# Optimization experiments

Measured on AMD Instinct MI355X. Metric: run time of the kernel, lower is better.

Reference implementation:

```python
import jax, jax.numpy as jnp
import numpy as np

NEG, NEG2, EPS, K = 0.01, 0.2, 1e-5, 10
B, N = 8, 2048

def lrelu(x, s):
    return jnp.where(x >= 0, x, s * x)

def bn_eval(x, g, b):
    # BatchNorm in eval mode with running_mean=0, running_var=1
    shp = [1] * x.ndim; shp[1] = -1
    return x * (g / np.sqrt(1.0 + EPS)).reshape(shp) + b.reshape(shp)

def conv1d(x, W, b):  # x [B,C,N], W [O,C]
    return jnp.einsum('bcn,oc->bon', x, W) + b[None, :, None]

def conv2d_1x1(x, W, b):  # x [B,C,N,K], W [O,C]
    return jnp.einsum('bcnk,oc->bonk', x, W) + b[None, :, None, None]

def edge_feats(x, k):
    # x: [B, d, N] -> [B, 2d, N, k]
    xt = jnp.swapaxes(x, 1, 2)                                   # [B,N,d]
    dist = (-2.0 * jnp.einsum('bnd,bdm->bnm', xt, x)
            + jnp.sum(xt ** 2, axis=2, keepdims=True)
            + jnp.sum(x ** 2, axis=1, keepdims=True))            # [B,N,N]
    idx = jnp.argsort(dist, axis=2)[:, :, 1:k + 1]               # [B,N,k]
    nbrs = jax.vmap(lambda xb, ib: xb[:, ib])(x, idx)            # [B,d,N,k]
    c = x[:, :, :, None]
    return jnp.concatenate([jnp.broadcast_to(c, nbrs.shape), nbrs - c], axis=1)

def edge_block(x, wc1, wcb1, bn1g, bn1b, wc2, wcb2, bn2g, bn2b,
               xc, xcb, xbng, xbnb, oW, ob):
    C = x.shape[1]
    ee = edge_feats(x, K)                                        # [B,2C,N,K]
    w = lrelu(bn_eval(conv2d_1x1(ee[:, C:], wc1, wcb1), bn1g, bn1b), NEG)
    w = lrelu(bn_eval(conv2d_1x1(w, wc2, wcb2), bn2g, bn2b), NEG)
    w = jax.nn.softmax(w, axis=-1)
    h = lrelu(bn_eval(conv2d_1x1(ee, xc, xcb), xbng, xbnb), NEG)
    # Conv2d(Fout, Fout, [1,K]): contract channels and neighbor axis
    return jnp.einsum('bcnj,ocj->bon', h * w, oW) + ob[None, :, None]

def adain(x, style, W, b):
    s = conv1d(style, W, b)
    g, be = jnp.split(s, 2, axis=1)
    m = jnp.mean(x, axis=2, keepdims=True)
    v = jnp.mean((x - m) ** 2, axis=2, keepdims=True)
    return g * ((x - m) * jax.lax.rsqrt(v + EPS)) + be

def _forward(z, x, hW1, hb1, hW2, hb2,
             e1_wc1, e1_wcb1, e1_bn1g, e1_bn1b, e1_wc2, e1_wcb2, e1_bn2g, e1_bn2b,
             e1_xc, e1_xcb, e1_xbng, e1_xbnb, e1_oW, e1_ob, a1_W, a1_b,
             e2_wc1, e2_wcb1, e2_bn1g, e2_bn1b, e2_wc2, e2_wcb2, e2_bn2g, e2_bn2b,
             e2_xc, e2_xcb, e2_xbng, e2_xbnb, e2_oW, e2_ob, a2_W, a2_b,
             gW1, gb1, gbn1g, gbn1b, gW2, gb2, gbn2g, gbn2b,
             tW1, tb1, tW2, tb2, tW3, tb3):
    st = jnp.swapaxes(jnp.concatenate([x, z], axis=-1), 1, 2)    # [B,3+nz,N]
    st = lrelu(conv1d(st, hW1, hb1), NEG)
    st = lrelu(conv1d(st, hW2, hb2), NEG)                        # [B,128,N]
    pc = jnp.swapaxes(x, 1, 2)                                   # [B,3,N]
    x1 = edge_block(pc, e1_wc1, e1_wcb1, e1_bn1g, e1_bn1b, e1_wc2, e1_wcb2,
                    e1_bn2g, e1_bn2b, e1_xc, e1_xcb, e1_xbng, e1_xbnb, e1_oW, e1_ob)
    x1 = adain(lrelu(x1, NEG2), st, a1_W, a1_b)                  # [B,64,N]
    x2 = edge_block(x1, e2_wc1, e2_wcb1, e2_bn1g, e2_bn1b, e2_wc2, e2_wcb2,
                    e2_bn2g, e2_bn2b, e2_xc, e2_xcb, e2_xbng, e2_xbnb, e2_oW, e2_ob)
    x2 = adain(lrelu(x2, NEG2), st, a2_W, a2_b)                  # [B,128,N]
    fg = jnp.max(x2, axis=2)                                     # [B,128]
    fg = lrelu(bn_eval(fg @ gW1.T + gb1, gbn1g, gbn1b), NEG)
    fg = lrelu(bn_eval(fg @ gW2.T + gb2, gbn2g, gbn2b), NEG)     # [B,512]
    fg = jnp.broadcast_to(fg[:, :, None], (fg.shape[0], 512, x2.shape[2]))
    feat = jnp.concatenate([fg, x2], axis=1)                     # [B,640,N]
    t = lrelu(conv1d(feat, tW1, tb1), NEG)
    t = lrelu(conv1d(t, tW2, tb2), NEG)
    t = conv1d(t, tW3, tb3)
    return jnp.swapaxes(t, 1, 2)                                 # [B,N,3]

_PARAM_SPECS = [
    ('hW1', (128, 131)), ('hb1', (128,)), ('hW2', (128, 128)), ('hb2', (128,)),
    ('e1_wc1', (32, 3)), ('e1_wcb1', (32,)), ('e1_bn1g', (32,)), ('e1_bn1b', (32,)),
    ('e1_wc2', (64, 32)), ('e1_wcb2', (64,)), ('e1_bn2g', (64,)), ('e1_bn2b', (64,)),
    ('e1_xc', (64, 6)), ('e1_xcb', (64,)), ('e1_xbng', (64,)), ('e1_xbnb', (64,)),
    ('e1_oW', (64, 64, 10)), ('e1_ob', (64,)), ('a1_W', (128, 128)), ('a1_b', (128,)),
    ('e2_wc1', (64, 64)), ('e2_wcb1', (64,)), ('e2_bn1g', (64,)), ('e2_bn1b', (64,)),
    ('e2_wc2', (128, 64)), ('e2_wcb2', (128,)), ('e2_bn2g', (128,)), ('e2_bn2b', (128,)),
    ('e2_xc', (128, 128)), ('e2_xcb', (128,)), ('e2_xbng', (128,)), ('e2_xbnb', (128,)),
    ('e2_oW', (128, 128, 10)), ('e2_ob', (128,)), ('a2_W', (256, 128)), ('a2_b', (256,)),
    ('gW1', (128, 128)), ('gb1', (128,)), ('gbn1g', (128,)), ('gbn1b', (128,)),
    ('gW2', (512, 128)), ('gb2', (512,)), ('gbn2g', (512,)), ('gbn2b', (512,)),
    ('tW1', (256, 640)), ('tb1', (256,)), ('tW2', (64, 256)), ('tb2', (64,)),
    ('tW3', (3, 64)), ('tb3', (3,)),
]

def setup_inputs() -> dict:
    key = jax.random.key(0)
    d = {
        'z': jax.random.normal(jax.random.fold_in(key, 1000), (B, N, 128), jnp.float32),
        'x': jax.random.normal(jax.random.fold_in(key, 1001), (B, N, 3), jnp.float32),
    }
    for i, (nm, sh) in enumerate(_PARAM_SPECS):
        v = 0.1 * jax.random.normal(jax.random.fold_in(key, i), sh, jnp.float32)
        if nm.endswith('g'):  # batchnorm gammas around 1
            v = v + 1.0
        d[nm] = v
    return d

def reference(z, x, hW1, hb1, hW2, hb2,
              e1_wc1, e1_wcb1, e1_bn1g, e1_bn1b, e1_wc2, e1_wcb2, e1_bn2g, e1_bn2b,
              e1_xc, e1_xcb, e1_xbng, e1_xbnb, e1_oW, e1_ob, a1_W, a1_b,
              e2_wc1, e2_wcb1, e2_bn1g, e2_bn1b, e2_wc2, e2_wcb2, e2_bn2g, e2_bn2b,
              e2_xc, e2_xcb, e2_xbng, e2_xbnb, e2_oW, e2_ob, a2_W, a2_b,
              gW1, gb1, gbn1g, gbn1b, gW2, gb2, gbn2g, gbn2b,
              tW1, tb1, tW2, tb2, tW3, tb3):
    return _forward(z, x, hW1, hb1, hW2, hb2,
                    e1_wc1, e1_wcb1, e1_bn1g, e1_bn1b, e1_wc2, e1_wcb2, e1_bn2g, e1_bn2b,
                    e1_xc, e1_xcb, e1_xbng, e1_xbnb, e1_oW, e1_ob, a1_W, a1_b,
                    e2_wc1, e2_wcb1, e2_bn1g, e2_bn1b, e2_wc2, e2_wcb2, e2_bn2g, e2_bn2b,
                    e2_xc, e2_xcb, e2_xbng, e2_xbnb, e2_oW, e2_ob, a2_W, a2_b,
                    gW1, gb1, gbn1g, gbn1b, gW2, gb2, gbn2g, gbn2b,
                    tW1, tb1, tW2, tb2, tW3, tb3)
```

## Files before the change

kernel.cpp:

```cpp
#include <hip/hip_runtime.h>
#include <math.h>

#define NPTS 2048
#define BATCH 8
#define KNB 10
#define NT (NPTS*KNB)

static __device__ __forceinline__ float lrelu(float x, float s){ return x >= 0.f ? x : s*x; }
static __device__ __forceinline__ double lrelu_d(double x, double s){ return x >= 0.0 ? x : s*x; }

template<int TM, int TN>
__global__ __launch_bounds__(256) void gemm_bn(
    const float* __restrict__ In, int ldn, size_t inBS, int koff,
    const float* __restrict__ W, int wstride, int wcol0,
    const float* __restrict__ cb, const float* __restrict__ bng, const float* __restrict__ bnb,
    const float* __restrict__ addBO, int addM,
    float* __restrict__ Out, int ldo, size_t outBS,
    int C, int act, float neg, int bbase)
{
  constexpr int RM = TM/16, RN = TN/16;
  __shared__ float As[16][TM+4];
  __shared__ float Bs[16][TN+4];
  const int b = bbase + blockIdx.z;
  const float* in = In + (size_t)b*inBS;
  float* outp = Out + (size_t)b*outBS;
  const int m0 = blockIdx.y*TM, n0 = blockIdx.x*TN;
  const int t = threadIdx.x;
  const int tmv = t>>4, tnv = t&15;
  float acc[RM][RN] = {};
  for (int k0=0; k0<C; k0+=16){
    #pragma unroll
    for (int s=0;s<RM;s++){
      const int i = t + s*256;
      const int k = i&15, m = i>>4;
      As[k][m] = W[(size_t)(m0+m)*wstride + wcol0 + k0 + k];
    }
    #pragma unroll
    for (int s=0;s<RN;s++){
      const int i = t + s*256;
      const int n = i & (TN-1), kk2 = i / TN;
      Bs[kk2][n] = in[(size_t)(koff + k0 + kk2)*ldn + n0 + n];
    }
    __syncthreads();
    #pragma unroll
    for (int kk=0;kk<16;kk++){
      float av[RM], bv[RN];
      #pragma unroll
      for (int s=0;s<RM/4;s++){
        float4 v = *(const float4*)&As[kk][tmv*RM + s*4];
        av[s*4]=v.x; av[s*4+1]=v.y; av[s*4+2]=v.z; av[s*4+3]=v.w;
      }
      #pragma unroll
      for (int s=0;s<RN/4;s++){
        float4 v = *(const float4*)&Bs[kk][tnv*RN + s*4];
        bv[s*4]=v.x; bv[s*4+1]=v.y; bv[s*4+2]=v.z; bv[s*4+3]=v.w;
      }
      #pragma unroll
      for (int i2=0;i2<RM;i2++)
        #pragma unroll
        for (int j2=0;j2<RN;j2++) acc[i2][j2] += av[i2]*bv[j2];
    }
    __syncthreads();
  }
  const float rs = 1.f/sqrtf(1.f + 1e-5f);
  #pragma unroll
  for (int i2=0;i2<RM;i2++){
    const int gm = m0 + tmv*RM + i2;
    float addv = cb ? cb[gm] : 0.f;
    if (addBO) addv += addBO[b*addM + gm];
    float sc = 1.f, bs = 0.f;
    if (bng){ sc = bng[gm]*rs; bs = bnb[gm]; }
    float* orow = outp + (size_t)gm*ldo + n0 + tnv*RN;
    #pragma unroll
    for (int j4=0;j4<RN/4;j4++){
      float4 o;
      float vv[4];
      #pragma unroll
      for (int q=0;q<4;q++){
        float v = acc[i2][j4*4+q] + addv;
        if (bng) v = v*sc + bs;
        if (act) v = lrelu(v, neg);
        vv[q] = v;
      }
      o.x=vv[0]; o.y=vv[1]; o.z=vv[2]; o.w=vv[3];
      *(float4*)&orow[j4*4] = o;
    }
  }
}

__global__ __launch_bounds__(256) void conv_gemm_exact(
    const float* __restrict__ in, const float* __restrict__ W, int wstride, int wcol0,
    const float* __restrict__ bias,
    float* __restrict__ out, int C, int M, int act, float neg)
{
  __shared__ float As[16][68];
  __shared__ float Bs[16][68];
  const int b = blockIdx.z;
  const int m0 = blockIdx.y*64, n0 = blockIdx.x*64;
  const int t = threadIdx.x;
  const int tm = t>>4, tn = t&15;
  float acc[4][4] = {};
  for (int k0 = 0; k0 < C; k0 += 16){
    #pragma unroll
    for (int i=0;i<4;i++){
      const int ii = t + i*256;
      const int k = ii&15, m = ii>>4;
      const int gm = m0+m, gk = k0+k;
      As[k][m] = (gm<M && gk<C) ? W[(size_t)gm*wstride + wcol0 + gk] : 0.f;
    }
    #pragma unroll
    for (int i=0;i<4;i++){
      const int ii = t + i*256;
      const int n = ii&63, k = ii>>6;
      const int gk = k0+k;
      Bs[k][n] = (gk<C) ? in[((size_t)b*C+gk)*NPTS + n0+n] : 0.f;
    }
    __syncthreads();
    #pragma unroll
    for (int k=0;k<16;k++){
      #pragma unroll
      for (int i=0;i<4;i++){
        const float a = As[k][tm*4+i];
        #pragma unroll
        for (int j=0;j<4;j++){
          acc[i][j] = __fadd_rn(acc[i][j], __fmul_rn(a, Bs[k][tn*4+j]));
        }
      }
    }
    __syncthreads();
  }
  #pragma unroll
  for (int i=0;i<4;i++){
    const int gm = m0 + tm*4 + i;
    if (gm < M){
      const float bv = bias ? bias[gm] : 0.f;
      #pragma unroll
      for (int j=0;j<4;j++){
        float v = __fadd_rn(acc[i][j], bv);
        if (act) v = (v >= 0.f) ? v : __fmul_rn(neg, v);
        out[((size_t)b*M+gm)*NPTS + n0 + tn*4 + j] = v;
      }
    }
  }
}

__global__ __launch_bounds__(256) void head1_exact(
    const float* __restrict__ x, const float* __restrict__ z,
    const float* __restrict__ W, const float* __restrict__ bias,
    float* __restrict__ outh)
{
  __shared__ float As[16][68];
  __shared__ float Bs[16][68];
  const int b = blockIdx.z;
  const int m0 = blockIdx.y*64, n0 = blockIdx.x*64;
  const int t = threadIdx.x;
  const int tm = t>>4, tn = t&15;
  float acc[4][4] = {};
  for (int k0 = 0; k0 < 144; k0 += 16){
    #pragma unroll
    for (int i=0;i<4;i++){
      const int ii = t + i*256;
      const int k = ii&15, m = ii>>4;
      const int gk = k0+k;
      As[k][m] = (gk<131) ? W[(size_t)(m0+m)*131 + gk] : 0.f;
    }
    #pragma unroll
    for (int i=0;i<4;i++){
      const int ii = t + i*256;
      const int k = ii&15, nn = ii>>4;
      const int gk = k0+k, gn = n0+nn;
      float v = 0.f;
      if (gk < 3)        v = x[((size_t)b*NPTS+gn)*3   + gk];
      else if (gk < 131) v = z[((size_t)b*NPTS+gn)*128 + (gk-3)];
      Bs[k][nn] = v;
    }
    __syncthreads();
    #pragma unroll
    for (int k=0;k<16;k++){
      #pragma unroll
      for (int i=0;i<4;i++){
        const float a = As[k][tm*4+i];
        #pragma unroll
        for (int j=0;j<4;j++){
          acc[i][j] = __fadd_rn(acc[i][j], __fmul_rn(a, Bs[k][tn*4+j]));
        }
      }
    }
    __syncthreads();
  }
  #pragma unroll
  for (int i=0;i<4;i++){
    const int gm = m0 + tm*4 + i;
    #pragma unroll
    for (int j=0;j<4;j++){
      float v = __fadd_rn(acc[i][j], bias[gm]);
      v = (v >= 0.f) ? v : __fmul_rn(0.01f, v);
      outh[((size_t)b*128+gm)*NPTS + n0 + tn*4 + j] = v;
    }
  }
}

__global__ __launch_bounds__(256) void norms3_f32(const float* __restrict__ Xn, float* __restrict__ XN)
{
  const int q = blockIdx.x*256 + threadIdx.x;
  const float* p = Xn + (size_t)q*3;
  float s = __fmul_rn(p[0],p[0]);
  s = __fadd_rn(s, __fmul_rn(p[1],p[1]));
  s = __fadd_rn(s, __fmul_rn(p[2],p[2]));
  XN[q] = s;
}

__global__ __launch_bounds__(256) void knn_part3(
    const float* __restrict__ Xn, const float* __restrict__ XN,
    double* __restrict__ topd, int* __restrict__ topi)
{
  const int t = threadIdx.x;
  const int qloc = t & 31, part = t >> 5;
  const int q = blockIdx.x*32 + qloc;
  const int b = q >> 11, n = q & (NPTS-1);
  const float* xb = Xn + (size_t)b*NPTS*3;
  const float qx = xb[(size_t)n*3+0], qy = xb[(size_t)n*3+1], qz = xb[(size_t)n*3+2];
  const float qn = XN[q];
  float td[11]; int ti[11];
  #pragma unroll
  for (int r=0;r<11;r++){ td[r] = 3.4e38f; ti[r] = 0x7fffffff; }
  const int m0 = part*(NPTS/8);
  for (int mm=0; mm<NPTS/8; mm++){
    const int m = m0 + mm;
    float dot = __fmul_rn(qx, xb[(size_t)m*3+0]);
    dot = __fadd_rn(dot, __fmul_rn(qy, xb[(size_t)m*3+1]));
    dot = __fadd_rn(dot, __fmul_rn(qz, xb[(size_t)m*3+2]));
    float dist = __fmul_rn(-2.f, dot);
    dist = __fadd_rn(dist, qn);
    dist = __fadd_rn(dist, XN[b*NPTS + m]);
    if (dist < td[10]){
      td[10] = dist; ti[10] = m;
      #pragma unroll
      for (int p=10;p>0;p--){
        if (td[p] < td[p-1]){
          float tf=td[p]; td[p]=td[p-1]; td[p-1]=tf;
          int   tt=ti[p]; ti[p]=ti[p-1]; ti[p-1]=tt;
        }
      }
    }
  }
  const size_t base = ((size_t)q*8 + part)*11;
  #pragma unroll
  for (int r=0;r<11;r++){ topd[base+r] = (double)td[r]; topi[base+r] = ti[r]; }
}

__global__ __launch_bounds__(256) void knn_merge_kernel(
    const double* __restrict__ topd, const int* __restrict__ topi, int* __restrict__ idxout)
{
  const int q = blockIdx.x*256 + threadIdx.x;
  double td[11]; int ti[11];
  #pragma unroll
  for (int r=0;r<11;r++){ td[r] = 1.0e308; ti[r] = 0x7fffffff; }
  const size_t base = (size_t)q*88;
  for (int s=0; s<88; s++){
    const double d = topd[base+s];
    const int  im = topi[base+s];
    if (d < td[10] || (d == td[10] && im < ti[10])){
      td[10] = d; ti[10] = im;
      #pragma unroll
      for (int p=10;p>0;p--){
        const bool sw = (td[p] < td[p-1]) || (td[p] == td[p-1] && ti[p] < ti[p-1]);
        if (sw){
          double tf=td[p]; td[p]=td[p-1]; td[p-1]=tf;
          int    tt=ti[p]; ti[p]=ti[p-1]; ti[p-1]=tt;
        }
      }
    }
  }
  #pragma unroll
  for (int j=0;j<KNB;j++) idxout[(size_t)q*KNB + j] = ti[j+1];
}

__global__ __launch_bounds__(256) void norms64_f32(const float* __restrict__ Xn, float* __restrict__ XN)
{
  const int q = blockIdx.x*256 + threadIdx.x;
  const float4* p4 = (const float4*)(Xn + (size_t)q*64);
  float s0=0.f,s1=0.f,s2=0.f,s3=0.f;
  #pragma unroll
  for (int d4=0; d4<16; d4++){
    float4 v = p4[d4];
    s0 += v.x*v.x; s1 += v.y*v.y; s2 += v.z*v.z; s3 += v.w*v.w;
  }
  XN[q] = (s0+s1)+(s2+s3);
}

__global__ __launch_bounds__(256) void knn_coarse(
    const float* __restrict__ Xn, const float* __restrict__ XN,
    float* __restrict__ topf, int* __restrict__ topi)
{
  const int t = threadIdx.x;
  const int qloc = t & 31, part = t >> 5;
  const int q = blockIdx.x*32 + qloc;
  const int b = q >> 11, n = q & (NPTS-1);
  const float* xb = Xn + (size_t)b*NPTS*64;
  float qv[64];
  {
    const float4* p4 = (const float4*)(xb + (size_t)n*64);
    #pragma unroll
    for (int d4=0; d4<16; d4++){ float4 v = p4[d4]; qv[d4*4]=v.x; qv[d4*4+1]=v.y; qv[d4*4+2]=v.z; qv[d4*4+3]=v.w; }
  }
  const float qn = XN[q];
  float td[16]; int ti[16];
  #pragma unroll
  for (int r=0;r<16;r++){ td[r] = 3.4e38f; ti[r] = 0x7fffffff; }
  const int m0 = part*(NPTS/8);
  #pragma unroll 2
  for (int mm=0; mm<NPTS/8; mm++){
    const int m = m0 + mm;
    const float4* c4 = (const float4*)(xb + (size_t)m*64);
    float d0=0.f,d1=0.f,d2=0.f,d3=0.f;
    #pragma unroll
    for (int d4=0; d4<16; d4++){
      float4 v = c4[d4];
      d0 += qv[d4*4+0]*v.x; d1 += qv[d4*4+1]*v.y;
      d2 += qv[d4*4+2]*v.z; d3 += qv[d4*4+3]*v.w;
    }
    const float dist = qn - 2.f*((d0+d1)+(d2+d3)) + XN[b*NPTS + m];
    if (dist < td[15]){
      td[15] = dist; ti[15] = m;
      #pragma unroll
      for (int p=15;p>0;p--){
        if (td[p] < td[p-1]){
          float tf=td[p]; td[p]=td[p-1]; td[p-1]=tf;
          int   tt=ti[p]; ti[p]=ti[p-1]; ti[p-1]=tt;
        }
      }
    }
  }
  const size_t base = ((size_t)q*8 + part)*16;
  #pragma unroll
  for (int r=0;r<16;r++){ topf[base+r] = td[r]; topi[base+r] = ti[r]; }
}

__global__ __launch_bounds__(256) void norms64d(const double* __restrict__ Xn, double* __restrict__ XN)
{
  const int q = blockIdx.x*256 + threadIdx.x;
  const double* p = Xn + (size_t)q*64;
  double s = 0.0;
  #pragma unroll
  for (int d=0; d<64; d++) s += p[d]*p[d];
  XN[q] = s;
}

__global__ __launch_bounds__(256) void knn_refine(
    const float* __restrict__ topf, const int* __restrict__ topi,
    const double* __restrict__ Xd, const double* __restrict__ XNd,
    int* __restrict__ idxout)
{
  const int q = blockIdx.x*256 + threadIdx.x;
  const int b = q >> 11;
  float tf[16]; int ti[16];
  #pragma unroll
  for (int r=0;r<16;r++){ tf[r] = 3.4e38f; ti[r] = 0x7fffffff; }
  const size_t base = (size_t)q*128;
  for (int s=0; s<128; s++){
    const float d = topf[base+s];
    const int  im = topi[base+s];
    if (d < tf[15] || (d == tf[15] && im < ti[15])){
      tf[15] = d; ti[15] = im;
      #pragma unroll
      for (int p=15;p>0;p--){
        const bool sw = (tf[p] < tf[p-1]) || (tf[p] == tf[p-1] && ti[p] < ti[p-1]);
        if (sw){
          float a=tf[p]; tf[p]=tf[p-1]; tf[p-1]=a;
          int   c=ti[p]; ti[p]=ti[p-1]; ti[p-1]=c;
        }
      }
    }
  }
  double qv[64];
  {
    const double2* p2 = (const double2*)(Xd + (size_t)q*64);
    #pragma unroll
    for (int d2=0; d2<32; d2++){ double2 v = p2[d2]; qv[d2*2]=v.x; qv[d2*2+1]=v.y; }
  }
  const double qn = XNd[q];
  double dd[11]; int di[11];
  #pragma unroll
  for (int r=0;r<11;r++){ dd[r] = 1.0e308; di[r] = 0x7fffffff; }
  for (int s=0; s<16; s++){
    const int m = ti[s];
    const double2* c2 = (const double2*)(Xd + ((size_t)(b*NPTS + m))*64);
    double d0=0.0,d1=0.0,d2s=0.0,d3=0.0;
    #pragma unroll
    for (int d4=0; d4<16; d4++){
      double2 va = c2[d4*2], vb = c2[d4*2+1];
      d0 += qv[d4*4+0]*va.x; d1 += qv[d4*4+1]*va.y;
      d2s+= qv[d4*4+2]*vb.x; d3 += qv[d4*4+3]*vb.y;
    }
    const double dot = (d0+d1)+(d2s+d3);
    const double dist = (qn - 2.0*dot) + XNd[b*NPTS + m];
    if (dist < dd[10] || (dist == dd[10] && m < di[10])){
      dd[10] = dist; di[10] = m;
      #pragma unroll
      for (int p=10;p>0;p--){
        const bool sw = (dd[p] < dd[p-1]) || (dd[p] == dd[p-1] && di[p] < di[p-1]);
        if (sw){
          double a=dd[p]; dd[p]=dd[p-1]; dd[p-1]=a;
          int    c=di[p]; di[p]=di[p-1]; di[p-1]=c;
        }
      }
    }
  }
  #pragma unroll
  for (int j=0;j<KNB;j++) idxout[(size_t)q*KNB + j] = di[j+1];
}

__global__ __launch_bounds__(512) void edge1_f64(
    const float* __restrict__ Xn, const int* __restrict__ idx,
    const float* __restrict__ wc1, const float* __restrict__ wcb1,
    const float* __restrict__ bn1g, const float* __restrict__ bn1b,
    const float* __restrict__ wc2, const float* __restrict__ wcb2,
    const float* __restrict__ bn2g, const float* __restrict__ bn2b,
    const float* __restrict__ xc,  const float* __restrict__ xcb,
    const float* __restrict__ xbng, const float* __restrict__ xbnb,
    const float* __restrict__ oWT, const float* __restrict__ ob,
    double* __restrict__ outX)
{
  __shared__ float wc1s[32][3];
  __shared__ float wc2s[64][33];
  __shared__ float xcs[64][7];
  __shared__ float wcb1s[32], wcb2s[64], xcbs[64];
  __shared__ double fs1d[32], fb1d[32], fs2d[64], fb2d[64], fsxd[64], fbxd[64];
  __shared__ float cenb[8][3], difb[8][3];
  __shared__ double w1bd[8][32];
  __shared__ float smw2[4096];
  __shared__ double hwbd[8][64];

  const int t = threadIdx.x;
  const double sq = sqrt(1.0 + 1e-5);
  for (int i=t; i<96;   i+=512) wc1s[i/3][i%3] = wc1[i];
  for (int i=t; i<2048; i+=512) wc2s[i/32][i%32] = wc2[i];
  for (int i=t; i<384;  i+=512) xcs[i/6][i%6] = xc[i];
  if (t < 32){ wcb1s[t]=wcb1[t]; fs1d[t]=(double)bn1g[t]/sq; fb1d[t]=(double)bn1b[t]; }
  else if (t < 96){ int o=t-32; wcb2s[o]=wcb2[o]; fs2d[o]=(double)bn2g[o]/sq; fb2d[o]=(double)bn2b[o]; }
  else if (t < 160){ int o=t-96; xcbs[o]=xcb[o]; fsxd[o]=(double)xbng[o]/sq; fbxd[o]=(double)xbnb[o]; }
  __syncthreads();

  const int wid = t>>6, lane = t&63;
  const int p = blockIdx.x*8 + wid;
  const int b = p >> 11, n = p & (NPTS-1);
  const float* xb = Xn + (size_t)b*NPTS*3;
  if (lane < 3) cenb[wid][lane] = xb[(size_t)n*3 + lane];
  __builtin_amdgcn_wave_barrier();
  const int* ip = idx + ((size_t)b*NPTS + n)*KNB;

  double w2r[KNB], hr[KNB];
  #pragma unroll
  for (int j=0;j<KNB;j++){
    const int id = ip[j];
    if (lane < 3) difb[wid][lane] = __fadd_rn(xb[(size_t)id*3 + lane], -cenb[wid][lane]);
    __builtin_amdgcn_wave_barrier();
    if (lane < 32){
      float s = __fmul_rn(wc1s[lane][0], difb[wid][0]);
      s = __fadd_rn(s, __fmul_rn(wc1s[lane][1], difb[wid][1]));
      s = __fadd_rn(s, __fmul_rn(wc1s[lane][2], difb[wid][2]));
      s = __fadd_rn(s, wcb1s[lane]);
      const double y = (double)s * fs1d[lane] + fb1d[lane];
      w1bd[wid][lane] = lrelu_d(y, 0.01);
    }
    __builtin_amdgcn_wave_barrier();
    {
      const int o = lane;
      double s2 = 0.0;
      #pragma unroll 8
      for (int m=0;m<32;m++) s2 += (double)wc2s[o][m] * w1bd[wid][m];
      s2 += (double)wcb2s[o];
      w2r[j] = lrelu_d(s2*fs2d[o] + fb2d[o], 0.01);
      float s3 = __fmul_rn(xcs[o][0], cenb[wid][0]);
      s3 = __fadd_rn(s3, __fmul_rn(xcs[o][1], cenb[wid][1]));
      s3 = __fadd_rn(s3, __fmul_rn(xcs[o][2], cenb[wid][2]));
      s3 = __fadd_rn(s3, __fmul_rn(xcs[o][3], difb[wid][0]));
      s3 = __fadd_rn(s3, __fmul_rn(xcs[o][4], difb[wid][1]));
      s3 = __fadd_rn(s3, __fmul_rn(xcs[o][5], difb[wid][2]));
      s3 = __fadd_rn(s3, xcbs[o]);
      hr[j] = lrelu_d((double)s3*fsxd[o] + fbxd[o], 0.01);
    }
    __builtin_amdgcn_wave_barrier();
  }

  double hw[KNB];
  {
    double mx = w2r[0];
    #pragma unroll
    for (int j=1;j<KNB;j++) mx = fmax(mx, w2r[j]);
    double ssum = 0.0;
    #pragma unroll
    for (int j=0;j<KNB;j++){ const double e = exp(w2r[j]-mx); w2r[j]=e; ssum+=e; }
    #pragma unroll
    for (int j=0;j<KNB;j++) hw[j] = hr[j]*(w2r[j]/ssum);
  }

  double acc = 0.0;
  #pragma unroll
  for (int j=0;j<KNB;j++){
    __syncthreads();
    for (int i=t; i<4096; i+=512) smw2[i] = oWT[(size_t)j*4096 + i];
    hwbd[wid][lane] = hw[j];
    __syncthreads();
    double s = 0.0;
    #pragma unroll 8
    for (int c=0;c<64;c++) s += (double)smw2[c*64 + lane]*hwbd[wid][c];
    acc += s;
  }
  outX[((size_t)b*64+lane)*NPTS + n] = acc + (double)ob[lane];
}

template<int CH>
__global__ void owt_kernel(const float* __restrict__ oW, float* __restrict__ oWT)
{
  const int i = blockIdx.x*256 + threadIdx.x;
  if (i < CH*CH*KNB){
    const int j  = i % KNB;
    const int c2 = (i / KNB) % CH;
    const int o  = i / (KNB*CH);
    oWT[((size_t)j*CH + c2)*CH + o] = oW[i];
  }
}

__global__ __launch_bounds__(256) void adain1_f64(
    double* __restrict__ X, const float* __restrict__ S)
{
  const int c = blockIdx.x, b = blockIdx.y;
  const int t = threadIdx.x;
  const size_t base = ((size_t)b*64 + c)*NPTS;
  __shared__ double red[256];
  double v[8];
  double s = 0.0;
  #pragma unroll
  for (int i=0;i<8;i++){
    double xv = X[base + t + i*256];
    xv = lrelu_d(xv, 0.2);
    v[i] = xv; s += xv;
  }
  red[t] = s; __syncthreads();
  for (int st=128; st>0; st>>=1){ if (t<st) red[t] += red[t+st]; __syncthreads(); }
  const double mean = red[0]/(double)NPTS;
  __syncthreads();
  double s2 = 0.0;
  #pragma unroll
  for (int i=0;i<8;i++){ const double d = v[i]-mean; s2 += d*d; }
  red[t] = s2; __syncthreads();
  for (int st=128; st>0; st>>=1){ if (t<st) red[t] += red[t+st]; __syncthreads(); }
  const double var  = red[0]/(double)NPTS;
  const double rstd = 1.0/sqrt(var + 1e-5);
  const float* g  = S + ((size_t)b*128 + c)*NPTS;
  const float* be = S + ((size_t)b*128 + 64 + c)*NPTS;
  #pragma unroll
  for (int i=0;i<8;i++){
    const int n = t + i*256;
    X[base+n] = (double)g[n]*((v[i]-mean)*rstd) + (double)be[n];
  }
}

__global__ __launch_bounds__(256) void transpose_cast64(
    const double* __restrict__ in, double* __restrict__ outT,
    float* __restrict__ outTf, float* __restrict__ outC)
{
  __shared__ double tile[64][65];
  const int b = blockIdx.y, n0 = blockIdx.x*64;
  const int t = threadIdx.x;
  for (int i=t; i<4096; i+=256){
    const int n=i&63, c=i>>6;
    const double v = in[((size_t)b*64+c)*NPTS + n0+n];
    tile[c][n] = v;
    outC[((size_t)b*64+c)*NPTS + n0+n] = (float)v;
  }
  __syncthreads();
  for (int i=t; i<4096; i+=256){
    const int c=i&63, n=i>>6;
    const double v = tile[c][n];
    outT [((size_t)b*NPTS+n0+n)*64 + c] = v;
    outTf[((size_t)b*NPTS+n0+n)*64 + c] = (float)v;
  }
}

__global__ __launch_bounds__(256) void kernelP(
    const float* __restrict__ x1c, const float* __restrict__ wc1,
    const float* __restrict__ xc,
    float* __restrict__ WCC, float* __restrict__ HCC)
{
  __shared__ float As[16][68];
  __shared__ float Bs[16][132];
  const int b = blockIdx.z;
  const int y = blockIdx.y;
  const int n0 = blockIdx.x*128;
  const int t = threadIdx.x;
  const int tm = t>>4, tn = t&15;
  float acc[4][8] = {};
  for (int k0=0; k0<64; k0+=16){
    #pragma unroll
    for (int s=0;s<4;s++){
      const int i = t + s*256;
      const int k = i&15, m = i>>4;
      float w;
      if (y == 0) w = wc1[(size_t)m*64 + k0 + k];
      else {
        const int c = (y-1)*64 + m;
        w = xc[(size_t)c*128 + k0 + k] - xc[(size_t)c*128 + 64 + k0 + k];
      }
      As[k][m] = w;
    }
    #pragma unroll
    for (int s=0;s<8;s++){
      const int i = t + s*256;
      const int n = i&127, kk = i>>7;
      Bs[kk][n] = x1c[((size_t)b*64 + k0 + kk)*NPTS + n0 + n];
    }
    __syncthreads();
    #pragma unroll
    for (int k=0;k<16;k++){
      float4 a4 = *(const float4*)&As[k][tm*4];
      const float av[4] = {a4.x, a4.y, a4.z, a4.w};
      #pragma unroll
      for (int j=0;j<8;j++){
        const float bv = Bs[k][tn + j*16];
        #pragma unroll
        for (int i2=0;i2<4;i2++) acc[i2][j] += av[i2]*bv;
      }
    }
    __syncthreads();
  }
  #pragma unroll
  for (int i2=0;i2<4;i2++){
    const int m = tm*4 + i2;
    #pragma unroll
    for (int j=0;j<8;j++){
      const int n = n0 + tn + j*16;
      if (y == 0) WCC[((size_t)b*64 + m)*NPTS + n] = acc[i2][j];
      else        HCC[((size_t)b*128 + (y-1)*64 + m)*NPTS + n] = acc[i2][j];
    }
  }
}

__global__ __launch_bounds__(256) void kernelA(
    const float* __restrict__ X1f, const int* __restrict__ IDX,
    const float* __restrict__ WCC,
    const float* __restrict__ wc1, const float* __restrict__ wcb1,
    const float* __restrict__ bn1g, const float* __restrict__ bn1b,
    float* __restrict__ W1, int bbase)
{
  __shared__ float wc1T[64*68];
  __shared__ float nbr[64*132];
  __shared__ int idx_l[128];
  const int b = bbase + blockIdx.z;
  const int n0 = blockIdx.x*128;
  const int t = threadIdx.x;
  const float* xb = X1f + (size_t)b*NPTS*64;

  if (t < 128){
    const int n = n0 + t;
    idx_l[t] = IDX[((size_t)b*NPTS + n/10)*KNB + (n%10)];
  }
  for (int i=t; i<4096; i+=256){
    const int k = i&63, m = i>>6;
    wc1T[k*68 + m] = wc1[(size_t)m*64 + k];
  }
  __syncthreads();
  const float4* xb4 = (const float4*)xb;
  #pragma unroll
  for (int r=0; r<8; r++){
    const int i = t + r*256;
    const int pos = i>>4, q4 = i&15;
    const float4 v = xb4[(size_t)idx_l[pos]*16 + q4];
    nbr[(q4*4+0)*132 + pos] = v.x;
    nbr[(q4*4+1)*132 + pos] = v.y;
    nbr[(q4*4+2)*132 + pos] = v.z;
    nbr[(q4*4+3)*132 + pos] = v.w;
  }
  __syncthreads();

  const int tm = t>>4, tn = t&15;
  float acc[4][8] = {};
  #pragma unroll 4
  for (int k=0;k<64;k++){
    float4 a4 = *(const float4*)&wc1T[k*68 + tm*4];
    const float av[4] = {a4.x, a4.y, a4.z, a4.w};
    #pragma unroll
    for (int j=0;j<8;j++){
      const float bv = nbr[k*132 + tn + j*16];
      #pragma unroll
      for (int i2=0;i2<4;i2++) acc[i2][j] += av[i2]*bv;
    }
  }
  const float rs = 1.f/sqrtf(1.f + 1e-5f);
  #pragma unroll
  for (int i2=0;i2<4;i2++){
    const int m = tm*4 + i2;
    const float bias = wcb1[m];
    const float sc = bn1g[m]*rs, bb = bn1b[m];
    #pragma unroll
    for (int j=0;j<8;j++){
      const int n = n0 + tn + j*16;
      const int p = n/10;
      float v = acc[i2][j] - WCC[((size_t)b*64 + m)*NPTS + p] + bias;
      v = lrelu(v*sc + bb, 0.01f);
      W1[((size_t)(b-bbase)*64 + m)*NT + n] = v;
    }
  }
}

#define C_WC2T 0
#define C_XCDT 4352
#define C_W1S  8704
#define C_NBRS 13952
#define C_TOT  19200
#define C_HW   0
#define C_OWL  5184

__global__ __launch_bounds__(256) void kernelC(
    const float* __restrict__ X1f, const int* __restrict__ IDX,
    const float* __restrict__ W1, const float* __restrict__ HCC,
    const float* __restrict__ wc2, const float* __restrict__ wcb2,
    const float* __restrict__ bn2g, const float* __restrict__ bn2b,
    const float* __restrict__ xc,  const float* __restrict__ xcb,
    const float* __restrict__ xbng, const float* __restrict__ xbnb,
    const float* __restrict__ oW, const float* __restrict__ ob,
    float* __restrict__ X2, int bbase)
{
  __shared__ float smC[C_TOT];
  __shared__ int idxC[80];
  const int b = bbase + blockIdx.z;
  const int n0 = blockIdx.x*80;
  const int p0 = n0/10;
  const int t = threadIdx.x;
  const float* xb = X1f + (size_t)b*NPTS*64;

  if (t < 80){
    const int n = n0 + t;
    idxC[t] = IDX[((size_t)b*NPTS + n/10)*KNB + (n%10)];
  }
  __syncthreads();

  const int tmv = t>>4, tnv = t&15, tnv5 = tnv*5;
  const int p_loc = tnv>>1, jh5 = (tnv&1)*5;
  const int o = t&127, phalf = t>>7;
  const float rs = 1.f/sqrtf(1.f + 1e-5f);
  float acc2[4] = {};

  for (int ch=0; ch<2; ch++){
    for (int i=t; i<4096; i+=256){
      const int k = i&63, cl = i>>6;
      smC[C_WC2T + k*68 + cl] = wc2[(size_t)(ch*64+cl)*64 + k];
      smC[C_XCDT + k*68 + cl] = xc[(size_t)(ch*64+cl)*128 + 64 + k];
    }
    for (int i=t; i<5120; i+=256){
      const int n = i%80, k = i/80;
      smC[C_W1S + k*82 + n] = W1[((size_t)(b-bbase)*64 + k)*NT + n0 + n];
    }
    {
      const float4* xb4 = (const float4*)xb;
      #pragma unroll
      for (int r=0;r<5;r++){
        const int i = t + r*256;
        const int pos = i>>4, q4 = i&15;
        const float4 v = xb4[(size_t)idxC[pos]*16 + q4];
        smC[C_NBRS + (q4*4+0)*82 + pos] = v.x;
        smC[C_NBRS + (q4*4+1)*82 + pos] = v.y;
        smC[C_NBRS + (q4*4+2)*82 + pos] = v.z;
        smC[C_NBRS + (q4*4+3)*82 + pos] = v.w;
      }
    }
    __syncthreads();

    float accw[4][5] = {}, acch[4][5] = {};
    #pragma unroll 2
    for (int k=0;k<64;k++){
      float4 a4 = *(const float4*)&smC[C_WC2T + k*68 + tmv*4];
      float4 x4 = *(const float4*)&smC[C_XCDT + k*68 + tmv*4];
      const float av[4] = {a4.x,a4.y,a4.z,a4.w};
      const float xv[4] = {x4.x,x4.y,x4.z,x4.w};
      float bw[5], bh[5];
      #pragma unroll
      for (int j=0;j<5;j++){
        bw[j] = smC[C_W1S  + k*82 + tnv5 + j];
        bh[j] = smC[C_NBRS + k*82 + tnv5 + j];
      }
      #pragma unroll
      for (int i2=0;i2<4;i2++)
        #pragma unroll
        for (int j=0;j<5;j++){ accw[i2][j]+=av[i2]*bw[j]; acch[i2][j]+=xv[i2]*bh[j]; }
    }

    float hwreg[4][5];
    #pragma unroll
    for (int i2=0;i2<4;i2++){
      const int c = ch*64 + tmv*4 + i2;
      const float s2 = bn2g[c]*rs, b2 = bn2b[c], cb2 = wcb2[c];
      const float sx = xbng[c]*rs, bx = xbnb[c], cbx = xcb[c];
      const float hcc = HCC[((size_t)b*128 + c)*NPTS + p0 + p_loc];
      float w2[5], hv[5];
      #pragma unroll
      for (int j=0;j<5;j++){
        w2[j] = lrelu((accw[i2][j] + cb2)*s2 + b2, 0.01f);
        hv[j] = lrelu((acch[i2][j] + hcc + cbx)*sx + bx, 0.01f);
      }
      float mx = w2[0];
      #pragma unroll
      for (int j=1;j<5;j++) mx = fmaxf(mx, w2[j]);
      mx = fmaxf(mx, __shfl_xor(mx, 1));
      float ssum = 0.f;
      #pragma unroll
      for (int j=0;j<5;j++){ w2[j] = expf(w2[j]-mx); ssum += w2[j]; }
      ssum += __shfl_xor(ssum, 1);
      const float inv = 1.f/ssum;
      #pragma unroll
      for (int j=0;j<5;j++) hwreg[i2][j] = hv[j]*(w2[j]*inv);
    }
    __syncthreads();

    #pragma unroll
    for (int i2=0;i2<4;i2++){
      const int cl = tmv*4 + i2;
      #pragma unroll
      for (int j=0;j<5;j++)
        smC[C_HW + p_loc*648 + cl*10 + jh5 + j] = hwreg[i2][j];
    }
    __syncthreads();

    for (int kc=0; kc<640; kc+=64){
      #pragma unroll
      for (int r=0;r<32;r++){
        const int i = t + r*256;
        const int oo = i>>6, kk = i&63;
        smC[C_OWL + oo*65 + kk] = oW[(size_t)oo*1280 + ch*640 + kc + kk];
      }
      __syncthreads();
      #pragma unroll 4
      for (int kk=0; kk<64; kk+=4){
        const float w0 = smC[C_OWL + o*65 + kk];
        const float w1v= smC[C_OWL + o*65 + kk+1];
        const float w2v= smC[C_OWL + o*65 + kk+2];
        const float w3v= smC[C_OWL + o*65 + kk+3];
        #pragma unroll
        for (int pp=0;pp<4;pp++){
          const float4 h4 = *(const float4*)&smC[C_HW + (phalf*4+pp)*648 + kc + kk];
          acc2[pp] += w0*h4.x + w1v*h4.y + w2v*h4.z + w3v*h4.w;
        }
      }
      __syncthreads();
    }
  }
  const float obv = ob[o];
  #pragma unroll
  for (int pp=0;pp<4;pp++)
    X2[((size_t)b*128 + o)*NPTS + p0 + phalf*4 + pp] = acc2[pp] + obv;
}

template<int CH>
__global__ __launch_bounds__(256) void adain_kernel(
    float* __restrict__ X, const float* __restrict__ S)
{
  const int c = blockIdx.x, b = blockIdx.y;
  const int t = threadIdx.x;
  const size_t base = ((size_t)b*CH + c)*NPTS;
  __shared__ float red[256];
  float v[8];
  float s = 0.f;
  #pragma unroll
  for (int i=0;i<8;i++){
    float xv = X[base + t + i*256];
    xv = lrelu(xv, 0.2f);
    v[i] = xv; s += xv;
  }
  red[t] = s; __syncthreads();
  for (int st=128; st>0; st>>=1){ if (t<st) red[t] += red[t+st]; __syncthreads(); }
  const float mean = red[0]*(1.f/NPTS);
  __syncthreads();
  float s2 = 0.f;
  #pragma unroll
  for (int i=0;i<8;i++){ const float d = v[i]-mean; s2 += d*d; }
  red[t] = s2; __syncthreads();
  for (int st=128; st>0; st>>=1){ if (t<st) red[t] += red[t+st]; __syncthreads(); }
  const float var  = red[0]*(1.f/NPTS);
  const float rstd = 1.f/sqrtf(var + 1e-5f);
  const float* g  = S + ((size_t)b*2*CH + c)*NPTS;
  const float* be = S + ((size_t)b*2*CH + CH + c)*NPTS;
  #pragma unroll
  for (int i=0;i<8;i++){
    const int n = t + i*256;
    X[base+n] = g[n]*((v[i]-mean)*rstd) + be[n];
  }
}

__global__ __launch_bounds__(256) void maxn_kernel(const float* __restrict__ X, float* __restrict__ FG)
{
  const int c = blockIdx.x, b = blockIdx.y;
  const int t = threadIdx.x;
  const float* p = X + ((size_t)b*128 + c)*NPTS;
  __shared__ float red[256];
  float m = -3.4e38f;
  for (int i=t; i<NPTS; i+=256) m = fmaxf(m, p[i]);
  red[t] = m; __syncthreads();
  for (int st=128; st>0; st>>=1){ if (t<st) red[t] = fmaxf(red[t], red[t+st]); __syncthreads(); }
  if (t == 0) FG[b*128+c] = red[0];
}

__global__ __launch_bounds__(512) void fc_kernel(
    const float* __restrict__ FG,
    const float* __restrict__ gW1, const float* __restrict__ gb1,
    const float* __restrict__ gbn1g, const float* __restrict__ gbn1b,
    const float* __restrict__ gW2, const float* __restrict__ gb2,
    const float* __restrict__ gbn2g, const float* __restrict__ gbn2b,
    const float* __restrict__ tW1, const float* __restrict__ tb1,
    float* __restrict__ FGP)
{
  const int b = blockIdx.x, t = threadIdx.x;
  __shared__ float fg[128], h1[128], h2[512];
  const float rs = 1.f/sqrtf(1.f + 1e-5f);
  if (t < 128) fg[t] = FG[b*128+t];
  __syncthreads();
  if (t < 128){
    float s = 0.f;
    for (int c=0;c<128;c++) s += gW1[t*128+c]*fg[c];
    s += gb1[t];
    s = s*(gbn1g[t]*rs) + gbn1b[t];
    h1[t] = lrelu(s, 0.01f);
  }
  __syncthreads();
  {
    float s = 0.f;
    for (int c=0;c<128;c++) s += gW2[t*128+c]*h1[c];
    s += gb2[t];
    s = s*(gbn2g[t]*rs) + gbn2b[t];
    h2[t] = lrelu(s, 0.01f);
  }
  __syncthreads();
  if (t < 256){
    float s = tb1[t];
    for (int c=0;c<512;c++) s += tW1[(size_t)t*640 + c]*h2[c];
    FGP[b*256+t] = s;
  }
}

__global__ __launch_bounds__(256) void t3_kernel(
    const float* __restrict__ T2, const float* __restrict__ tW3,
    const float* __restrict__ tb3, float* __restrict__ outp)
{
  __shared__ float w[192];
  const int t = threadIdx.x;
  if (t < 192) w[t] = tW3[t];
  __syncthreads();
  const int b = blockIdx.y;
  const int n = blockIdx.x*256 + t;
  float a0 = tb3[0], a1 = tb3[1], a2 = tb3[2];
  for (int c=0;c<64;c++){
    const float v = T2[((size_t)b*64+c)*NPTS + n];
    a0 += w[c]*v; a1 += w[64+c]*v; a2 += w[128+c]*v;
  }
  float* op = outp + ((size_t)b*NPTS + n)*3;
  op[0]=a0; op[1]=a1; op[2]=a2;
}

extern "C" void kernel_launch(void* const* d_in, const int* in_sizes, int n_in,
                              void* d_out, int out_size, void* d_ws, size_t ws_size,
                              hipStream_t stream)
{
  (void)in_sizes; (void)n_in; (void)out_size; (void)ws_size;
  const float* z    = (const float*)d_in[0];
  const float* x    = (const float*)d_in[1];
  const float* hW1  = (const float*)d_in[2];
  const float* hb1  = (const float*)d_in[3];
  const float* hW2  = (const float*)d_in[4];
  const float* hb2  = (const float*)d_in[5];
  const float* e1_wc1 = (const float*)d_in[6];
  const float* e1_wcb1= (const float*)d_in[7];
  const float* e1_bn1g= (const float*)d_in[8];
  const float* e1_bn1b= (const float*)d_in[9];
  const float* e1_wc2 = (const float*)d_in[10];
  const float* e1_wcb2= (const float*)d_in[11];
  const float* e1_bn2g= (const float*)d_in[12];
  const float* e1_bn2b= (const float*)d_in[13];
  const float* e1_xc  = (const float*)d_in[14];
  const float* e1_xcb = (const float*)d_in[15];
  const float* e1_xbng= (const float*)d_in[16];
  const float* e1_xbnb= (const float*)d_in[17];
  const float* e1_oW  = (const float*)d_in[18];
  const float* e1_ob  = (const float*)d_in[19];
  const float* a1_W   = (const float*)d_in[20];
  const float* a1_b   = (const float*)d_in[21];
  const float* e2_wc1 = (const float*)d_in[22];
  const float* e2_wcb1= (const float*)d_in[23];
  const float* e2_bn1g= (const float*)d_in[24];
  const float* e2_bn1b= (const float*)d_in[25];
  const float* e2_wc2 = (const float*)d_in[26];
  const float* e2_wcb2= (const float*)d_in[27];
  const float* e2_bn2g= (const float*)d_in[28];
  const float* e2_bn2b= (const float*)d_in[29];
  const float* e2_xc  = (const float*)d_in[30];
  const float* e2_xcb = (const float*)d_in[31];
  const float* e2_xbng= (const float*)d_in[32];
  const float* e2_xbnb= (const float*)d_in[33];
  const float* e2_oW  = (const float*)d_in[34];
  const float* e2_ob  = (const float*)d_in[35];
  const float* a2_W   = (const float*)d_in[36];
  const float* a2_b   = (const float*)d_in[37];
  const float* gW1    = (const float*)d_in[38];
  const float* gb1    = (const float*)d_in[39];
  const float* gbn1g  = (const float*)d_in[40];
  const float* gbn1b  = (const float*)d_in[41];
  const float* gW2    = (const float*)d_in[42];
  const float* gb2    = (const float*)d_in[43];
  const float* gbn2g  = (const float*)d_in[44];
  const float* gbn2b  = (const float*)d_in[45];
  const float* tW1    = (const float*)d_in[46];
  const float* tb1    = (const float*)d_in[47];
  const float* tW2    = (const float*)d_in[48];
  const float* tb2    = (const float*)d_in[49];
  const float* tW3    = (const float*)d_in[50];
  const float* tb3    = (const float*)d_in[51];
  float* out = (float*)d_out;
  float* ws  = (float*)d_ws;

  size_t off = 0;
  float*  ST    = ws + off; off += (size_t)BATCH*128*NPTS;
  float*  Sbuf  = ws + off; off += (size_t)BATCH*256*NPTS;
  float*  X1f   = ws + off; off += (size_t)BATCH*NPTS*64;
  float*  X2    = ws + off; off += (size_t)BATCH*128*NPTS;
  float*  T1    = ws + off; off += (size_t)BATCH*256*NPTS;
  float*  T2    = ws + off; off += (size_t)BATCH*64*NPTS;
  int*    IDX   = (int*)(ws + off); off += (size_t)BATCH*NPTS*KNB;
  float*  OW1T  = ws + off; off += (size_t)64*64*KNB;
  float*  XN3f  = ws + off; off += (size_t)BATCH*NPTS;
  double* XN64  = (double*)(ws + off); off += (size_t)2*BATCH*NPTS;
  float*  FG    = ws + off; off += (size_t)BATCH*128;
  float*  FGP   = ws + off; off += (size_t)BATCH*256;
  off = (off + 1) & ~(size_t)1;
  double* X1_64 = (double*)(ws + off); off += (size_t)2*BATCH*64*NPTS;
  double* X1T64 = (double*)(ws + off); off += (size_t)2*BATCH*NPTS*64;

  double* TOPD  = (double*)T1;
  int*    TOPI  = (int*)Sbuf;
  float*  TOPF  = (float*)X1_64;
  int*    TOPI2 = (int*)T1;
  float*  X1c   = Sbuf;
  float*  WCC   = Sbuf + 1048576;
  float*  HCC   = Sbuf + 2097152;
  float*  W1    = T1;

  owt_kernel<64><<<(64*64*KNB+255)/256, 256, 0, stream>>>(e1_oW, OW1T);

  head1_exact<<<dim3(32,2,8), 256, 0, stream>>>(x, z, hW1, hb1, T1);
  conv_gemm_exact<<<dim3(32,2,8), 256, 0, stream>>>(T1, hW2, 128, 0, hb2, ST, 128, 128, 1, 0.01f);

  norms3_f32<<<64, 256, 0, stream>>>(x, XN3f);
  knn_part3<<<512, 256, 0, stream>>>(x, XN3f, TOPD, TOPI);
  knn_merge_kernel<<<64, 256, 0, stream>>>(TOPD, TOPI, IDX);
  edge1_f64<<<2048, 512, 0, stream>>>(
      x, IDX, e1_wc1, e1_wcb1, e1_bn1g, e1_bn1b, e1_wc2, e1_wcb2, e1_bn2g, e1_bn2b,
      e1_xc, e1_xcb, e1_xbng, e1_xbnb, OW1T, e1_ob, X1_64);
  conv_gemm_exact<<<dim3(32,2,8), 256, 0, stream>>>(ST, a1_W, 128, 0, a1_b, Sbuf, 128, 128, 0, 0.f);
  adain1_f64<<<dim3(64,8), 256, 0, stream>>>(X1_64, Sbuf);

  transpose_cast64<<<dim3(32,8), 256, 0, stream>>>(X1_64, X1T64, X1f, X1c);

  norms64_f32<<<64, 256, 0, stream>>>(X1f, XN3f);
  norms64d<<<64, 256, 0, stream>>>(X1T64, XN64);
  knn_coarse<<<512, 256, 0, stream>>>(X1f, XN3f, TOPF, TOPI2);
  knn_refine<<<64, 256, 0, stream>>>(TOPF, TOPI2, X1T64, XN64, IDX);

  kernelP<<<dim3(16,3,8), 256, 0, stream>>>(X1c, e2_wc1, e2_xc, WCC, HCC);
  for (int lb=0; lb<4; lb++){
    const int bbase = lb*2;
    kernelA<<<dim3(NT/128,1,2), 256, 0, stream>>>(
        X1f, IDX, WCC, e2_wc1, e2_wcb1, e2_bn1g, e2_bn1b, W1, bbase);
    kernelC<<<dim3(NT/80,1,2), 256, 0, stream>>>(
        X1f, IDX, W1, HCC, e2_wc2, e2_wcb2, e2_bn2g, e2_bn2b,
        e2_xc, e2_xcb, e2_xbng, e2_xbnb, e2_oW, e2_ob, X2, bbase);
  }

  gemm_bn<128,128><<<dim3(NPTS/128,2,8), 256, 0, stream>>>(
      ST, NPTS, (size_t)128*NPTS, 0, a2_W, 128, 0, a2_b, nullptr, nullptr, nullptr, 0,
      Sbuf, NPTS, (size_t)256*NPTS, 128, 0, 0.f, 0);
  adain_kernel<128><<<dim3(128,8), 256, 0, stream>>>(X2, Sbuf);

  maxn_kernel<<<dim3(128,8), 256, 0, stream>>>(X2, FG);
  fc_kernel<<<8, 512, 0, stream>>>(FG, gW1, gb1, gbn1g, gbn1b, gW2, gb2, gbn2g, gbn2b, tW1, tb1, FGP);
  gemm_bn<128,128><<<dim3(NPTS/128,2,8), 256, 0, stream>>>(
      X2, NPTS, (size_t)128*NPTS, 0, tW1, 640, 512, nullptr, nullptr, nullptr, FGP, 256,
      T1, NPTS, (size_t)256*NPTS, 128, 1, 0.01f, 0);
  gemm_bn<64,128><<<dim3(NPTS/128,1,8), 256, 0, stream>>>(
      T1, NPTS, (size_t)256*NPTS, 0, tW2, 256, 0, tb2, nullptr, nullptr, nullptr, 0,
      T2, NPTS, (size_t)64*NPTS, 256, 1, 0.01f, 0);
  t3_kernel<<<dim3(8,8), 256, 0, stream>>>(T2, tW3, tb3, out);
}
```

Before: 1.710 ms.

## Stage candidate point tiles in shared memory for coarse kNN scan

The coarse kNN kernel now loads 64-point candidate tiles cooperatively into LDS, along with their norms, and all 256 threads reuse them. Before, each thread streamed candidate vectors straight from global memory. Each thread keeps one query and one of eight interleaved candidate partitions (rows m where m mod 8 equals its partition id). Per-partition top-16 lists therefore hold different candidates than before, but the refine stage still sees the full set. This cuts redundant global and L2 traffic at the cost of two barriers per tile and 17 KB of LDS per block.

```diff
diff --git a/kernel.cpp b/kernel.cpp
--- a/kernel.cpp
+++ b/kernel.cpp
@@ -293,46 +293,62 @@
     const float* __restrict__ Xn, const float* __restrict__ XN,
     float* __restrict__ topf, int* __restrict__ topi)
 {
-  const int t = threadIdx.x;
-  const int qloc = t & 31, part = t >> 5;
-  const int q = blockIdx.x*32 + qloc;
-  const int b = q >> 11, n = q & (NPTS-1);
+  __shared__ float Cs[64][68];
+  __shared__ float xns[64];
+  const int t = threadIdx.x;
+  const int tq = t>>3, p = t&7;
+  const int q0 = blockIdx.x*32;
+  const int b  = q0 >> 11;
+  const int gq = q0 + tq;
+  const int nloc = (q0 & (NPTS-1)) + tq;
   const float* xb = Xn + (size_t)b*NPTS*64;
   float qv[64];
   {
-    const float4* p4 = (const float4*)(xb + (size_t)n*64);
+    const float4* p4 = (const float4*)(xb + (size_t)nloc*64);
     #pragma unroll
     for (int d4=0; d4<16; d4++){ float4 v = p4[d4]; qv[d4*4]=v.x; qv[d4*4+1]=v.y; qv[d4*4+2]=v.z; qv[d4*4+3]=v.w; }
   }
-  const float qn = XN[q];
+  const float qn = XN[gq];
   float td[16]; int ti[16];
   #pragma unroll
   for (int r=0;r<16;r++){ td[r] = 3.4e38f; ti[r] = 0x7fffffff; }
-  const int m0 = part*(NPTS/8);
-  #pragma unroll 2
-  for (int mm=0; mm<NPTS/8; mm++){
-    const int m = m0 + mm;
-    const float4* c4 = (const float4*)(xb + (size_t)m*64);
-    float d0=0.f,d1=0.f,d2=0.f,d3=0.f;
-    #pragma unroll
-    for (int d4=0; d4<16; d4++){
-      float4 v = c4[d4];
-      d0 += qv[d4*4+0]*v.x; d1 += qv[d4*4+1]*v.y;
-      d2 += qv[d4*4+2]*v.z; d3 += qv[d4*4+3]*v.w;
-    }
-    const float dist = qn - 2.f*((d0+d1)+(d2+d3)) + XN[b*NPTS + m];
-    if (dist < td[15]){
-      td[15] = dist; ti[15] = m;
-      #pragma unroll
-      for (int p=15;p>0;p--){
-        if (td[p] < td[p-1]){
-          float tf=td[p]; td[p]=td[p-1]; td[p-1]=tf;
-          int   tt=ti[p]; ti[p]=ti[p-1]; ti[p-1]=tt;
+
+  for (int m0=0; m0<NPTS; m0+=64){
+    __syncthreads();
+    #pragma unroll
+    for (int s=0;s<4;s++){
+      const int i = t + s*256;
+      const int row = i>>4, f4 = i&15;
+      float4 v = *(const float4*)(xb + (size_t)(m0+row)*64 + f4*4);
+      *(float4*)&Cs[row][f4*4] = v;
+    }
+    if (t < 64) xns[t] = XN[b*NPTS + m0 + t];
+    __syncthreads();
+    #pragma unroll
+    for (int jj=0;jj<8;jj++){
+      const int row = jj*8 + p;
+      float d0=0.f,d1=0.f,d2=0.f,d3=0.f;
+      #pragma unroll
+      for (int k4=0;k4<16;k4++){
+        float4 v = *(const float4*)&Cs[row][k4*4];
+        d0 += qv[k4*4+0]*v.x; d1 += qv[k4*4+1]*v.y;
+        d2 += qv[k4*4+2]*v.z; d3 += qv[k4*4+3]*v.w;
+      }
+      const float dist = qn - 2.f*((d0+d1)+(d2+d3)) + xns[row];
+      const int m = m0 + row;
+      if (dist < td[15]){
+        td[15] = dist; ti[15] = m;
+        #pragma unroll
+        for (int pp=15;pp>0;pp--){
+          if (td[pp] < td[pp-1]){
+            float tf=td[pp]; td[pp]=td[pp-1]; td[pp-1]=tf;
+            int   tt=ti[pp]; ti[pp]=ti[pp-1]; ti[pp-1]=tt;
+          }
         }
       }
     }
   }
-  const size_t base = ((size_t)q*8 + part)*16;
+  const size_t base = ((size_t)gq*8 + p)*16;
   #pragma unroll
   for (int r=0;r<16;r++){ topf[base+r] = td[r]; topi[base+r] = ti[r]; }
 }
```

New measurement: 1.579 ms. 7.7% less time.
